# Kernel optimization log

Measured on AMD Instinct MI355X. Metric: run time of the kernel, lower is better.

The kernel has to match this reference:

```python
import jax, jax.numpy as jnp
import numpy as np

NEG = -1.0e30  # log-space 'zero' that is safe in fp32
EPS = 1e-7     # keras.backend.ctc_batch_cost epsilon


def setup_inputs() -> dict:
    key = jax.random.key(0)
    k1, k2 = jax.random.split(key)
    B, T, C, L = 256, 512, 256, 128
    # y_pred are post-softmax probabilities, as expected by ctc_batch_cost
    logits = jax.random.normal(k1, (B, T, C), dtype=jnp.float32)
    y_pred = jax.nn.softmax(logits, axis=-1)
    # labels in [0, C-1): never equal to blank index C-1
    y_true = jax.random.randint(k2, (B, L), 0, C - 1, dtype=jnp.int32)
    return {"y_true": y_true, "y_pred": y_pred}


def _ctc_batch_cost(y_true, y_pred):
    """Faithful keras.backend.ctc_batch_cost with full input/label lengths.

    y_true: [B, L] int labels (no blanks). y_pred: [B, T, C] probabilities.
    Blank index = C - 1 (TF v1 ctc_loss convention). Returns [B, 1] loss.
    """
    B, T, C = y_pred.shape
    L = y_true.shape[1]
    blank = C - 1
    S = 2 * L + 1  # extended label: blank, l0, blank, l1, ..., blank

    logp = jnp.log(y_pred + EPS)                                # [B, T, C]
    ext = jnp.full((B, S), blank, dtype=y_true.dtype).at[:, 1::2].set(y_true)
    # per-(t, s) log prob of the extended symbol
    lp = jnp.take_along_axis(logp, ext[:, None, :].astype(jnp.int32), axis=2)  # [B, T, S]

    # skip transition s-2 -> s allowed iff s >= 2, ext[s] != blank, ext[s] != ext[s-2]
    ext_m2 = jnp.pad(ext, ((0, 0), (2, 0)), constant_values=blank)[:, :S]
    skip = (ext != blank) & (ext != ext_m2) & (jnp.arange(S)[None, :] >= 2)

    # alpha init at t=0: only s=0 (blank) and s=1 (first label) reachable
    alpha0 = jnp.where(jnp.arange(S)[None, :] < 2, lp[:, 0, :], NEG)  # [B, S]

    def step(alpha, lp_t):
        p1 = jnp.pad(alpha, ((0, 0), (1, 0)), constant_values=NEG)[:, :S]
        p2 = jnp.pad(alpha, ((0, 0), (2, 0)), constant_values=NEG)[:, :S]
        a = jnp.logaddexp(alpha, p1)
        a = jnp.logaddexp(a, jnp.where(skip, p2, NEG))
        return a + lp_t, None

    lp_time_major = jnp.moveaxis(lp, 1, 0)  # [T, B, S]
    alpha, _ = jax.lax.scan(step, alpha0, lp_time_major[1:])
    # total log-likelihood ends at last blank or last label
    loss = -jnp.logaddexp(alpha[:, S - 1], alpha[:, S - 2])    # [B]
    return loss[:, None]                                        # [B, 1]


def reference(y_true, y_pred):
    # CTCLayer.call computes ctc_batch_cost with input_length = T, label_length = L
    # for every batch row, adds it as a loss, and passes y_pred through. The
    # compute of interest is the loss itself, returned here as [B, 1].
    return _ctc_batch_cost(y_true, y_pred)
```

## Files before the change

### kernel.cpp

```cpp
#include <hip/hip_runtime.h>
#include <math.h>


namespace {
constexpr int Bn = 256;
constexpr int Tn = 512;
constexpr int Cn = 256;
constexpr int Ln = 128;
constexpr int D  = 32;
constexpr float EPSf = 1e-7f;
constexpr float LN2f = 0.69314718055994530942f;
constexpr int   TGT  = 60;
}

typedef float f4 __attribute__((ext_vector_type(4)));

#define GLOAD(dst, p) \
    asm volatile("global_load_dwordx4 %0, %1, off" : "=v"(dst) : "v"(p))
#define WAITP(dst) \
    asm volatile("s_waitcnt vmcnt(31)" : "+v"(dst))
#define WAIT0(dst) \
    asm volatile("s_waitcnt vmcnt(0)" : "+v"(dst))

__device__ __forceinline__ float bpf(int idx4, float v) {
    return __int_as_float(__builtin_amdgcn_ds_bpermute(idx4, __float_as_int(v)));
}

__global__ __launch_bounds__(64, 1)
void ctc_fwd(const int* __restrict__ y_true,
             const float* __restrict__ y_pred,
             float* __restrict__ out)
{
    const int b    = blockIdx.x;
    const int lane = threadIdx.x;

    const int* yt = y_true + b * Ln;
    const int l0 = yt[2 * lane];
    const int l1 = yt[2 * lane + 1];
    const int lm = (lane > 0) ? yt[2 * lane - 1] : -1;
    const float sk1 = (lane > 0 && l0 != lm) ? 1.0f : 0.0f;
    const float sk3 = (l1 != l0) ? 1.0f : 0.0f;
    const float lzm = (lane > 0) ? 1.0f : 0.0f;

    const int i0 = (l0 >> 2) << 2;
    const int i1 = (l1 >> 2) << 2;
    const bool s0a = l0 & 1, s0b = l0 & 2;
    const bool s1a = l1 & 1, s1b = l1 & 2;

    float a0 = (lane == 0) ? 1.0f : 0.0f;
    float a1 = 0.0f, a2 = 0.0f, a3 = 0.0f, a4 = 0.0f;
    int Eacc = 0;

    auto step = [&](f4 r) {
        float x0 = bpf(i0, r.x), x1 = bpf(i0, r.y);
        float x2 = bpf(i0, r.z), x3 = bpf(i0, r.w);
        float y0 = bpf(i1, r.x), y1 = bpf(i1, r.y);
        float y2 = bpf(i1, r.z), y3 = bpf(i1, r.w);
        float v0 = s0b ? (s0a ? x3 : x2) : (s0a ? x1 : x0);
        float v1 = s1b ? (s1a ? y3 : y2) : (s1a ? y1 : y0);
        float bb = __int_as_float(
            __builtin_amdgcn_readlane(__float_as_int(r.w), 63));

        float n  = __shfl_up(a3, 1) * lzm;
        const float Pb = bb + EPSf;
        const float P0 = v0 + EPSf;
        const float P1 = v1 + EPSf;
        const float na0 = (a0 + n) * Pb;
        const float na1 = fmaf(sk1, n,  a1 + a0) * P0;
        const float na2 = (a2 + a1) * Pb;
        const float na3 = fmaf(sk3, a1, a3 + a2) * P1;
        const float na4 = (a4 + a3) * Pb;
        a0 = na0; a1 = na1; a2 = na2; a3 = na3; a4 = na4;
    };

    auto rescale = [&]() {
        float m = fmaxf(fmaxf(fmaxf(a0, a1), fmaxf(a2, a3)), a4);
        #pragma unroll
        for (int off = 32; off >= 1; off >>= 1)
            m = fmaxf(m, __shfl_xor(m, off));
        int e;
        (void)frexpf(m, &e);
        const int shift = TGT - e;
        a0 = ldexpf(a0, shift);
        a1 = ldexpf(a1, shift);
        a2 = ldexpf(a2, shift);
        a3 = ldexpf(a3, shift);
        a4 = ldexpf(a4, shift);
        Eacc -= shift;
    };

    const float* p = y_pred + (size_t)b * Tn * Cn + lane * 4;
    f4 buf[D];

    #pragma unroll
    for (int j = 0; j < D; ++j) { GLOAD(buf[j], p); p += Cn; }

    for (int c = 0; c < Tn - D; c += D) {
        #pragma unroll
        for (int j = 0; j < D; ++j) {
            WAITP(buf[j]);
            step(buf[j]);
            GLOAD(buf[j], p); p += Cn;
            if ((j & 7) == 7) rescale();
        }
    }
    #pragma unroll
    for (int j = 0; j < D; ++j) {
        WAIT0(buf[j]);
        step(buf[j]);
        if ((j & 7) == 7) rescale();
    }

    if (lane == 63) {
        const float s = a3 + a4;
        out[b] = -LN2f * (log2f(s) + (float)Eacc);
    }
}

extern "C" void kernel_launch(void* const* d_in, const int* in_sizes, int n_in,
                              void* d_out, int out_size, void* d_ws, size_t ws_size,
                              hipStream_t stream) {
    const int*   y_true = (const int*)  d_in[0];
    const float* y_pred = (const float*)d_in[1];
    float* out = (float*)d_out;
    (void)in_sizes; (void)n_in; (void)out_size; (void)d_ws; (void)ws_size;
    ctc_fwd<<<dim3(Bn), dim3(64), 0, stream>>>(y_true, y_pred, out);
}
```

Baseline: 210.3 us.

## Gather label probabilities through LDS ring buffer, software-pipelined one step

Each step's eight ds_bpermute gathers plus select logic are replaced by a vectorized store of the timestep's row into a 4-slot LDS ring and two indexed LDS reads. The reads for step t-1 are issued before the store of step t, so LDS latency overlaps the recurrence. Rescaling drops from every 8 steps to twice per 32, and the target exponent is raised to 100 with a pre-scaled initial alpha to leave more headroom. The gain relies on a single wavefront making LDS ordering implicit without barriers, and the sparser rescaling risks underflow if probabilities shrink faster than the headroom allows.

After: 198.6 us. 1.06x faster.

```diff
diff --git a/kernel.cpp b/kernel.cpp
--- a/kernel.cpp
+++ b/kernel.cpp
@@ -10,7 +10,7 @@
 constexpr int D  = 32;
 constexpr float EPSf = 1e-7f;
 constexpr float LN2f = 0.69314718055994530942f;
-constexpr int   TGT  = 60;
+constexpr int   TGT  = 100;
 }
 
 typedef float f4 __attribute__((ext_vector_type(4)));
@@ -22,8 +22,8 @@
 #define WAIT0(dst) \
     asm volatile("s_waitcnt vmcnt(0)" : "+v"(dst))
 
-__device__ __forceinline__ float bpf(int idx4, float v) {
-    return __int_as_float(__builtin_amdgcn_ds_bpermute(idx4, __float_as_int(v)));
+__device__ __forceinline__ float rdl63(float v) {
+    return __int_as_float(__builtin_amdgcn_readlane(__float_as_int(v), 63));
 }
 
 __global__ __launch_bounds__(64, 1)
@@ -34,6 +34,8 @@
     const int b    = blockIdx.x;
     const int lane = threadIdx.x;
 
+    __shared__ __align__(16) float lds[4 * Cn];
+
     const int* yt = y_true + b * Ln;
     const int l0 = yt[2 * lane];
     const int l1 = yt[2 * lane + 1];
@@ -42,29 +44,15 @@
     const float sk3 = (l1 != l0) ? 1.0f : 0.0f;
     const float lzm = (lane > 0) ? 1.0f : 0.0f;
 
-    const int i0 = (l0 >> 2) << 2;
-    const int i1 = (l1 >> 2) << 2;
-    const bool s0a = l0 & 1, s0b = l0 & 2;
-    const bool s1a = l1 & 1, s1b = l1 & 2;
+    float a0 = (lane == 0) ? 0x1p100f : 0.0f;
+    float a1 = 0.0f, a2 = 0.0f, a3 = 0.0f, a4 = 0.0f;
+    int Eacc = -100;
 
-    float a0 = (lane == 0) ? 1.0f : 0.0f;
-    float a1 = 0.0f, a2 = 0.0f, a3 = 0.0f, a4 = 0.0f;
-    int Eacc = 0;
-
-    auto step = [&](f4 r) {
-        float x0 = bpf(i0, r.x), x1 = bpf(i0, r.y);
-        float x2 = bpf(i0, r.z), x3 = bpf(i0, r.w);
-        float y0 = bpf(i1, r.x), y1 = bpf(i1, r.y);
-        float y2 = bpf(i1, r.z), y3 = bpf(i1, r.w);
-        float v0 = s0b ? (s0a ? x3 : x2) : (s0a ? x1 : x0);
-        float v1 = s1b ? (s1a ? y3 : y2) : (s1a ? y1 : y0);
-        float bb = __int_as_float(
-            __builtin_amdgcn_readlane(__float_as_int(r.w), 63));
-
-        float n  = __shfl_up(a3, 1) * lzm;
-        const float Pb = bb + EPSf;
-        const float P0 = v0 + EPSf;
-        const float P1 = v1 + EPSf;
+    auto step = [&](float rb, float r0, float r1) {
+        float n = __shfl_up(a3, 1) * lzm;
+        const float Pb = rb + EPSf;
+        const float P0 = r0 + EPSf;
+        const float P1 = r1 + EPSf;
         const float na0 = (a0 + n) * Pb;
         const float na1 = fmaf(sk1, n,  a1 + a0) * P0;
         const float na2 = (a2 + a1) * Pb;
@@ -89,26 +77,60 @@
         Eacc -= shift;
     };
 
-    const float* p = y_pred + (size_t)b * Tn * Cn + lane * 4;
+    const f4* p = (const f4*)(y_pred + (size_t)b * Tn * Cn) + lane;
     f4 buf[D];
+    #pragma unroll
+    for (int j = 0; j < D; ++j) { GLOAD(buf[j], p); p += Cn / 4; }
+
+    float bold = 0.0f;
 
     #pragma unroll
-    for (int j = 0; j < D; ++j) { GLOAD(buf[j], p); p += Cn; }
+    for (int j = 0; j < D; ++j) {
+        WAITP(buf[j]);
+        const float bnew = rdl63(buf[j].w);
+        float r0n = 0.0f, r1n = 0.0f;
+        if (j >= 1) {
+            r0n = lds[((j - 1) & 3) * Cn + l0];
+            r1n = lds[((j - 1) & 3) * Cn + l1];
+        }
+        ((f4*)lds)[(j & 3) * (Cn / 4) + lane] = buf[j];
+        GLOAD(buf[j], p); p += Cn / 4;
+        if (j >= 1) step(bold, r0n, r1n);
+        bold = bnew;
+        if (j == 16) rescale();
+    }
 
-    for (int c = 0; c < Tn - D; c += D) {
+    for (int c = D; c < Tn - D; c += D) {
         #pragma unroll
         for (int j = 0; j < D; ++j) {
             WAITP(buf[j]);
-            step(buf[j]);
-            GLOAD(buf[j], p); p += Cn;
-            if ((j & 7) == 7) rescale();
+            const float bnew = rdl63(buf[j].w);
+            const float r0n = lds[((j - 1) & 3) * Cn + l0];
+            const float r1n = lds[((j - 1) & 3) * Cn + l1];
+            ((f4*)lds)[(j & 3) * (Cn / 4) + lane] = buf[j];
+            GLOAD(buf[j], p); p += Cn / 4;
+            step(bold, r0n, r1n);
+            bold = bnew;
+            if (j == 0 || j == 16) rescale();
         }
     }
+
     #pragma unroll
     for (int j = 0; j < D; ++j) {
         WAIT0(buf[j]);
-        step(buf[j]);
-        if ((j & 7) == 7) rescale();
+        const float bnew = rdl63(buf[j].w);
+        const float r0n = lds[((j - 1) & 3) * Cn + l0];
+        const float r1n = lds[((j - 1) & 3) * Cn + l1];
+        ((f4*)lds)[(j & 3) * (Cn / 4) + lane] = buf[j];
+        step(bold, r0n, r1n);
+        bold = bnew;
+        if (j == 0 || j == 16) rescale();
+    }
+
+    {
+        const float r0n = lds[3 * Cn + l0];
+        const float r1n = lds[3 * Cn + l1];
+        step(bold, r0n, r1n);
     }
 
     if (lane == 63) {
```
